# Performance work log

Hardware: AMD Instinct MI355X
Metric: run time of the kernel (lower is better)

## Reference

```python
import jax, jax.numpy as jnp
import numpy as np

B, N, E_PER = 512, 256, 8192          # graphs, nodes per graph, edges per graph
FIN, H, K, FOUT = 128, 32, 16, 10     # in_channels, hidden, num clusters, out_channels
EPS = 1e-15


def setup_inputs() -> dict:
    key = jax.random.key(0)
    ks = jax.random.split(key, 12)
    x = jax.random.normal(ks[0], (B * N, FIN), jnp.float32)
    # intra-graph random edges, then offset into the global node index space
    src = jax.random.randint(ks[1], (B, E_PER), 0, N)
    dst = jax.random.randint(ks[2], (B, E_PER), 0, N)
    offs = (jnp.arange(B) * N)[:, None]
    edge_index = jnp.stack([(src + offs).reshape(-1), (dst + offs).reshape(-1)]).astype(jnp.int64)
    batch = jnp.repeat(jnp.arange(B), N).astype(jnp.int64)

    def lin(k, fin, fout):
        return (jax.random.normal(k, (fin, fout), jnp.float32) / np.sqrt(fin)).astype(jnp.float32)

    params = {
        'W_lin1': lin(ks[3], FIN, H), 'b_lin1': jnp.zeros((H,), jnp.float32),
        'W_rel1': lin(ks[4], H, H), 'b_rel1': jnp.zeros((H,), jnp.float32),
        'W_root1': lin(ks[5], H, H),
        'W_pool': lin(ks[6], H, K), 'b_pool': jnp.zeros((K,), jnp.float32),
        'W_rel2': lin(ks[7], H, H), 'b_rel2': jnp.zeros((H,), jnp.float32),
        'W_root2': lin(ks[8], H, H),
        'W_lin2': lin(ks[9], H, H), 'b_lin2': jnp.zeros((H,), jnp.float32),
        'W_lin3': lin(ks[10], H, FOUT), 'b_lin3': jnp.zeros((FOUT,), jnp.float32),
    }
    return {'x': x, 'edge_index': edge_index, 'batch': batch, **params}


def _densify(x, edge_index, batch):
    """to_dense_adj + to_dense_batch: [total,F] -> [B,N,F], [B,N,N], [B,N]."""
    n_total = x.shape[0]
    counts = jax.ops.segment_sum(jnp.ones((n_total,), jnp.int32), batch, num_segments=B)
    offsets = jnp.concatenate([jnp.zeros((1,), jnp.int32), jnp.cumsum(counts)[:-1]])
    pos = jnp.arange(n_total) - offsets[batch]            # position of node inside its graph
    eb = batch[edge_index[0]]                             # graph id of each edge
    adj = jnp.zeros((B, N, N), jnp.float32).at[eb, pos[edge_index[0]], pos[edge_index[1]]].add(1.0)
    xd = jnp.zeros((B, N, x.shape[1]), jnp.float32).at[batch, pos].set(x)
    mask = jnp.zeros((B, N), jnp.float32).at[batch, pos].set(1.0)
    return xd, adj, mask


def _dense_graph_conv(x, adj, W_rel, b_rel, W_root):
    # PyG DenseGraphConv(aggr='add'): lin_rel(adj @ x) + lin_root(x)
    return jnp.einsum('bnm,bmh,hk->bnk', adj, x, W_rel) + b_rel + x @ W_root


def _dense_mincut_pool(x, adj, s, mask):
    s = jax.nn.softmax(s, axis=-1)
    x = x * mask[..., None]
    s = s * mask[..., None]
    out = jnp.einsum('bnk,bnh->bkh', s, x)                        # s^T x
    out_adj = jnp.einsum('bnk,bnm,bmj->bkj', s, adj, s)           # s^T A s
    mincut_num = jnp.einsum('bkk->b', out_adj)
    d_flat = adj.sum(-1)                                          # degree
    mincut_den = jnp.einsum('bnk,bn,bnk->b', s, d_flat, s)        # trace(s^T D s)
    mincut_loss = jnp.mean(-(mincut_num / mincut_den))
    ss = jnp.einsum('bnk,bnj->bkj', s, s)
    ss_norm = jnp.linalg.norm(ss, axis=(-1, -2), keepdims=True)
    i_s = jnp.eye(K, dtype=jnp.float32)
    ortho_loss = jnp.mean(jnp.linalg.norm(ss / ss_norm - i_s / jnp.sqrt(jnp.float32(K)), axis=(-1, -2)))
    # zero diagonal, symmetric degree normalization
    diag_mask = 1.0 - i_s
    out_adj = out_adj * diag_mask
    d = jnp.sqrt(out_adj.sum(-1))[:, None, :] + EPS               # [B,1,K]
    out_adj = out_adj / d / jnp.swapaxes(d, 1, 2)
    return out, out_adj, mincut_loss, ortho_loss


def reference(x, edge_index, batch, W_lin1, b_lin1, W_rel1, b_rel1, W_root1,
              W_pool, b_pool, W_rel2, b_rel2, W_root2, W_lin2, b_lin2, W_lin3, b_lin3):
    xd, adj, mask = _densify(x, edge_index, batch)
    h = xd @ W_lin1 + b_lin1                                      # lin1
    h = _dense_graph_conv(h, adj, W_rel1, b_rel1, W_root1)        # conv1
    s2 = h @ W_pool + b_pool                                      # pool2
    h, adj_p, mincut_loss2, ortho_loss2 = _dense_mincut_pool(h, adj, s2, mask)
    h = _dense_graph_conv(h, adj_p, W_rel2, b_rel2, W_root2)      # conv2
    h = h.sum(axis=1)                                             # readout sum over clusters
    h = jax.nn.relu(h @ W_lin2 + b_lin2)
    h = h @ W_lin3 + b_lin3
    return jax.nn.log_softmax(h, axis=-1), mincut_loss2, ortho_loss2
```

## Files before the change

kernel.cpp:

```cpp
#include <hip/hip_runtime.h>

#define NB 512
#define NN 256
#define EPG 8192
#define FINC 128

typedef float f32x4 __attribute__((ext_vector_type(4)));
typedef short s16x8 __attribute__((ext_vector_type(8)));

__device__ __forceinline__ float bf2f(unsigned short u) {
  union { unsigned int i; float f; } x; x.i = ((unsigned int)u) << 16; return x.f;
}
__device__ __forceinline__ unsigned short f2bf(float f) {
  union { float f; unsigned int i; } x; x.f = f;
  unsigned int r = x.i + 0x7fffu + ((x.i >> 16) & 1u);
  return (unsigned short)(r >> 16);
}
__device__ __forceinline__ short ftrunc_bf(float f) {
  union { float f; unsigned int i; } x; x.f = f;
  return (short)(x.i >> 16);
}

struct Params {
  const void* x; const void* ei;
  const void *wl1, *bl1, *wr1, *br1, *wro1, *wp, *bp;
  const void *wr2, *br2, *wro2, *wl2, *bl2, *wl3, *bl3;
  float* out; float* ws;
};

__device__ __forceinline__ bool detect_bf16(const void* p) {
  const unsigned short* pw = (const unsigned short*)p;
  int sane = 0;
  for (int i = 0; i < 64; ++i) {
    unsigned e = (pw[i] >> 7) & 0xFFu;
    sane += (e > 96u && e < 132u) ? 1 : 0;
  }
  return sane >= 56;
}
__device__ __forceinline__ bool detect_i64(const void* p) {
  const int* pi = (const int*)p + EPG;
  int ok = 0;
  for (int i = 0; i < 32; ++i) ok += (pi[i] >= 256 && pi[i] < 512) ? 1 : 0;
  return ok < 24;
}
__device__ __forceinline__ float ldf(const void* p, int i, bool bf) {
  return bf ? bf2f(((const unsigned short*)p)[i]) : ((const float*)p)[i];
}

#define SMEM_TOTAL 81920

__global__ __launch_bounds__(1024, 8) void mincut_main(Params P) {
  extern __shared__ char smem[];
  const int t = threadIdx.x;
  const int b = blockIdx.x;

  const bool BF  = detect_bf16(P.wr1);
  const bool I64 = detect_i64(P.ei);

  float* pbuf   = (float*)(smem + 0);
  float* oadjb  = (float*)(smem + 2048);
  float* ssb    = (float*)(smem + 3072);
  float* qbuf   = (float*)(smem + 4096);
  float* ddb    = (float*)(smem + 6144);
  float* h2b    = (float*)(smem + 6208);
  float* rb     = (float*)(smem + 8256);
  float* yb     = (float*)(smem + 8384);
  float* lgb    = (float*)(smem + 8512);
  float* scr    = (float*)(smem + 8704);
  float* rel2f  = (float*)(smem + 9216);
  float* root2f = (float*)(smem + 13312);
  float* lin2f  = (float*)(smem + 17408);
  float* lin3f  = (float*)(smem + 21504);
  float* brel2f = (float*)(smem + 22784);
  float* blin2f = (float*)(smem + 22912);
  float* blin3f = (float*)(smem + 23040);
  float* pbufH  = (float*)(smem + 24576);
  float* pbufL  = (float*)(smem + 26624);
  float* oadjH  = (float*)(smem + 28672);
  float* oadjL  = (float*)(smem + 29696);
  float* ssA    = (float*)(smem + 30720);
  float* ssX    = (float*)(smem + 31744);
  unsigned short* h0T  = (unsigned short*)(smem + 33792);
  unsigned short* yTl  = (unsigned short*)(smem + 33792);
  unsigned short* h1Th = (unsigned short*)(smem + 33792);
  unsigned short* w1t  = (unsigned short*)(smem + 50688);
  unsigned short* zT   = (unsigned short*)(smem + 50688);
  unsigned short* sTh  = (unsigned short*)(smem + 50688);
  unsigned short* sTl  = (unsigned short*)(smem + 59136);
  unsigned short* wrelTh = (unsigned short*)(smem + 67584);
  unsigned short* wrelTl = (unsigned short*)(smem + 70144);
  unsigned short* wrootT = (unsigned short*)(smem + 72704);
  float* blin1f = (float*)(smem + 75264);
  unsigned short* yTh = (unsigned short*)(smem + 67584);
  unsigned short* taT = (unsigned short*)(smem + 67584);
  unsigned short* wpoolTh = (unsigned short*)(smem + 76032);
  unsigned short* wpoolTl = (unsigned short*)(smem + 77184);
  unsigned short* m1Th    = (unsigned short*)(smem + 78336);
  unsigned short* m1Tl    = (unsigned short*)(smem + 79488);
  float*          scrE    = (float*)(smem + 79488);
  unsigned short* m2Th    = (unsigned short*)(smem + 80640);
  float*          bMf     = (float*)(smem + 81792);
  unsigned short* brel1h  = (unsigned short*)(smem + 81856);

  const int wv = t >> 6, lane = t & 63;
  const int lm = lane & 15, quad = lane >> 4;
  const int mbase = wv * 16;

  {
    uint4 z = {0u, 0u, 0u, 0u};
    for (int i = t; i < 2112; i += 1024) ((uint4*)smem)[i] = z;
  }
  for (int e = t; e < 4096; e += 1024) {
    int k = e >> 5, c = e & 31;
    w1t[c * 136 + k] = f2bf(ldf(P.wl1, e, BF));
  }
  {
    int k = t >> 5, c = t & 31;
    float wr = ldf(P.wr1, t, BF);
    unsigned short hi = f2bf(wr);
    wrelTh[c * 40 + k] = hi;
    wrelTl[c * 40 + k] = f2bf(wr - bf2f(hi));
    wrootT[c * 40 + k] = f2bf(ldf(P.wro1, t, BF));
  }
  if (t < 512) {
    int m = t >> 4, c = t & 15;
    float w = ldf(P.wp, t, BF);
    unsigned short hi = f2bf(w);
    wpoolTh[c * 36 + m] = hi;
    wpoolTl[c * 36 + m] = f2bf(w - bf2f(hi));
  }
  if (t < 32) { blin1f[t] = ldf(P.bl1, t, BF); brel1h[t] = f2bf(ldf(P.br1, t, BF)); }
  __syncthreads();

  if (I64) {
    const uint4* s4 = (const uint4*)((const long long*)P.ei + (size_t)b * EPG) + t * 4;
    const uint4* d4 = (const uint4*)((const long long*)P.ei + (size_t)NB * EPG + (size_t)b * EPG) + t * 4;
    #pragma unroll
    for (int i = 0; i < 4; ++i) {
      uint4 a = s4[i], c = d4[i];
      unsigned n0 = (a.x & 255u) * 264u + (c.x & 255u);
      unsigned n1 = (a.z & 255u) * 264u + (c.z & 255u);
      atomicAdd((unsigned int*)(smem + ((n0 >> 3) << 2)), 1u << ((n0 & 7u) * 4u));
      atomicAdd((unsigned int*)(smem + ((n1 >> 3) << 2)), 1u << ((n1 & 7u) * 4u));
    }
  } else {
    const uint4* s4 = (const uint4*)((const int*)P.ei + (size_t)b * EPG) + t * 2;
    const uint4* d4 = (const uint4*)((const int*)P.ei + (size_t)NB * EPG + (size_t)b * EPG) + t * 2;
    #pragma unroll
    for (int i = 0; i < 2; ++i) {
      uint4 a = s4[i], c = d4[i];
      unsigned n0 = (a.x & 255u) * 264u + (c.x & 255u);
      unsigned n1 = (a.y & 255u) * 264u + (c.y & 255u);
      unsigned n2 = (a.z & 255u) * 264u + (c.z & 255u);
      unsigned n3 = (a.w & 255u) * 264u + (c.w & 255u);
      atomicAdd((unsigned int*)(smem + ((n0 >> 3) << 2)), 1u << ((n0 & 7u) * 4u));
      atomicAdd((unsigned int*)(smem + ((n1 >> 3) << 2)), 1u << ((n1 & 7u) * 4u));
      atomicAdd((unsigned int*)(smem + ((n2 >> 3) << 2)), 1u << ((n2 & 7u) * 4u));
      atomicAdd((unsigned int*)(smem + ((n3 >> 3) << 2)), 1u << ((n3 & 7u) * 4u));
    }
  }

  {
    f32x4 acc[2] = {{0.f,0.f,0.f,0.f},{0.f,0.f,0.f,0.f}};
    const size_t node = (size_t)(b * 256 + mbase + lm);
    #pragma unroll
    for (int ks = 0; ks < 4; ++ks) {
      const int k0 = ks * 32 + quad * 8;
      s16x8 a;
      if (BF) {
        a = *(const s16x8*)((const unsigned short*)P.x + node * 128 + k0);
      } else {
        const float* xp = (const float*)P.x + node * 128 + k0;
        f32x4 v0 = *(const f32x4*)xp;
        f32x4 v1 = *(const f32x4*)(xp + 4);
        #pragma unroll
        for (int j = 0; j < 4; ++j) { a[j] = (short)f2bf(v0[j]); a[4 + j] = (short)f2bf(v1[j]); }
      }
      #pragma unroll
      for (int ct = 0; ct < 2; ++ct) {
        s16x8 bh = *(const s16x8*)(w1t + (ct * 16 + lm) * 136 + k0);
        acc[ct] = __builtin_amdgcn_mfma_f32_16x16x32_bf16(a, bh, acc[ct], 0, 0, 0);
      }
    }
    #pragma unroll
    for (int ct = 0; ct < 2; ++ct) {
      const int c = ct * 16 + lm;
      float bias = blin1f[c];
      #pragma unroll
      for (int r = 0; r < 4; ++r)
        h0T[c * 264 + mbase + quad * 4 + r] = f2bf(acc[ct][r] + bias);
    }
  }

  if (wv == 2 || wv == 3) {
    const int mb = (wv - 2) * 16;
    s16x8 Ah, Al;
    #pragma unroll
    for (int j = 0; j < 8; ++j) {
      int k = quad * 8 + j;
      Ah[j] = (short)wrelTh[k * 40 + mb + lm];
      Al[j] = (short)wrelTl[k * 40 + mb + lm];
    }
    s16x8 Bh, Bl;
    ((uint2*)&Bh)[0] = *(const uint2*)(wpoolTh + lm * 36 + quad * 8);
    ((uint2*)&Bh)[1] = *(const uint2*)(wpoolTh + lm * 36 + quad * 8 + 4);
    ((uint2*)&Bl)[0] = *(const uint2*)(wpoolTl + lm * 36 + quad * 8);
    ((uint2*)&Bl)[1] = *(const uint2*)(wpoolTl + lm * 36 + quad * 8 + 4);
    f32x4 acc = {0.f, 0.f, 0.f, 0.f};
    acc = __builtin_amdgcn_mfma_f32_16x16x32_bf16(Ah, Bh, acc, 0, 0, 0);
    acc = __builtin_amdgcn_mfma_f32_16x16x32_bf16(Al, Bh, acc, 0, 0, 0);
    acc = __builtin_amdgcn_mfma_f32_16x16x32_bf16(Ah, Bl, acc, 0, 0, 0);
    #pragma unroll
    for (int r = 0; r < 4; ++r) {
      int m = mb + quad * 4 + r;
      unsigned short hi = f2bf(acc[r]);
      m1Th[lm * 36 + m] = hi;
      m1Tl[lm * 36 + m] = f2bf(acc[r] - bf2f(hi));
    }
  }
  if (wv == 4 || wv == 5) {
    const int mb = (wv - 4) * 16;
    s16x8 Ah;
    #pragma unroll
    for (int j = 0; j < 8; ++j) Ah[j] = (short)wrootT[(quad * 8 + j) * 40 + mb + lm];
    s16x8 Bh, Bl;
    ((uint2*)&Bh)[0] = *(const uint2*)(wpoolTh + lm * 36 + quad * 8);
    ((uint2*)&Bh)[1] = *(const uint2*)(wpoolTh + lm * 36 + quad * 8 + 4);
    ((uint2*)&Bl)[0] = *(const uint2*)(wpoolTl + lm * 36 + quad * 8);
    ((uint2*)&Bl)[1] = *(const uint2*)(wpoolTl + lm * 36 + quad * 8 + 4);
    f32x4 acc = {0.f, 0.f, 0.f, 0.f};
    acc = __builtin_amdgcn_mfma_f32_16x16x32_bf16(Ah, Bh, acc, 0, 0, 0);
    acc = __builtin_amdgcn_mfma_f32_16x16x32_bf16(Ah, Bl, acc, 0, 0, 0);
    #pragma unroll
    for (int r = 0; r < 4; ++r) m2Th[lm * 36 + (mb + quad * 4 + r)] = f2bf(acc[r]);
  }
  if (wv == 6 && lane < 16) {
    float acc = ldf(P.bp, lane, BF);
    #pragma unroll 8
    for (int m = 0; m < 32; ++m)
      acc += bf2f(brel1h[m]) * (bf2f(wpoolTh[lane * 36 + m]) + bf2f(wpoolTl[lane * 36 + m]));
    bMf[lane] = acc;
  }
  __syncthreads();

  f32x4 racc[2] = {{0.f,0.f,0.f,0.f},{0.f,0.f,0.f,0.f}};
  f32x4 yacc = {0.f,0.f,0.f,0.f}, macc = {0.f,0.f,0.f,0.f};
  {
    s16x8 Ah;
    #pragma unroll
    for (int j = 0; j < 8; ++j) Ah[j] = (short)h0T[(quad * 8 + j) * 264 + mbase + lm];
    f32x4 zacc[2] = {{0.f,0.f,0.f,0.f},{0.f,0.f,0.f,0.f}};
    #pragma unroll
    for (int ct = 0; ct < 2; ++ct) {
      const int c = ct * 16 + lm;
      s16x8 brh = *(const s16x8*)(wrelTh + c * 40 + quad * 8);
      s16x8 brl = *(const s16x8*)(wrelTl + c * 40 + quad * 8);
      s16x8 bro = *(const s16x8*)(wrootT + c * 40 + quad * 8);
      zacc[ct] = __builtin_amdgcn_mfma_f32_16x16x32_bf16(Ah, brh, zacc[ct], 0, 0, 0);
      zacc[ct] = __builtin_amdgcn_mfma_f32_16x16x32_bf16(Ah, brl, zacc[ct], 0, 0, 0);
      racc[ct] = __builtin_amdgcn_mfma_f32_16x16x32_bf16(Ah, bro, racc[ct], 0, 0, 0);
    }
    s16x8 Bm1h, Bm1l, Bm2;
    ((uint2*)&Bm1h)[0] = *(const uint2*)(m1Th + lm * 36 + quad * 8);
    ((uint2*)&Bm1h)[1] = *(const uint2*)(m1Th + lm * 36 + quad * 8 + 4);
    ((uint2*)&Bm1l)[0] = *(const uint2*)(m1Tl + lm * 36 + quad * 8);
    ((uint2*)&Bm1l)[1] = *(const uint2*)(m1Tl + lm * 36 + quad * 8 + 4);
    ((uint2*)&Bm2)[0]  = *(const uint2*)(m2Th + lm * 36 + quad * 8);
    ((uint2*)&Bm2)[1]  = *(const uint2*)(m2Th + lm * 36 + quad * 8 + 4);
    yacc = __builtin_amdgcn_mfma_f32_16x16x32_bf16(Ah, Bm1h, yacc, 0, 0, 0);
    yacc = __builtin_amdgcn_mfma_f32_16x16x32_bf16(Ah, Bm1l, yacc, 0, 0, 0);
    macc = __builtin_amdgcn_mfma_f32_16x16x32_bf16(Ah, Bm2, macc, 0, 0, 0);
    #pragma unroll
    for (int ct = 0; ct < 2; ++ct)
      #pragma unroll
      for (int r = 0; r < 4; ++r)
        zT[(ct * 16 + lm) * 264 + mbase + quad * 4 + r] = f2bf(zacc[ct][r]);
  }
  __syncthreads();

  #pragma unroll
  for (int r = 0; r < 4; ++r) {
    int node = mbase + quad * 4 + r;
    unsigned short hi = f2bf(yacc[r]);
    yTh[lm * 264 + node] = hi;
    yTl[lm * 264 + node] = f2bf(yacc[r] - bf2f(hi));
  }
  __syncthreads();

  f32x4 h1v[2], sval;
  {
    f32x4 h1acc[2] = { racc[0], racc[1] };
    f32x4 lacc = macc;
    unsigned dsum = 0;
    const char* arow = smem + (mbase + lm) * 132;
    #pragma unroll
    for (int ks = 0; ks < 8; ++ks) {
      unsigned d = *(const unsigned int*)(arow + ks * 16 + quad * 4);
      unsigned v = (d & 0x0F0F0F0Fu) + ((d >> 4) & 0x0F0F0F0Fu);
      dsum += (v * 0x01010101u) >> 24;
      s16x8 af;
      #pragma unroll
      for (int j = 0; j < 8; ++j) af[j] = ftrunc_bf((float)((d >> (4 * j)) & 15u));
      const int v0 = ks * 32 + quad * 8;
      #pragma unroll
      for (int ct = 0; ct < 2; ++ct) {
        s16x8 bz = *(const s16x8*)(zT + (ct * 16 + lm) * 264 + v0);
        h1acc[ct] = __builtin_amdgcn_mfma_f32_16x16x32_bf16(af, bz, h1acc[ct], 0, 0, 0);
      }
      s16x8 byh = *(const s16x8*)(yTh + lm * 264 + v0);
      s16x8 byl = *(const s16x8*)(yTl + lm * 264 + v0);
      lacc = __builtin_amdgcn_mfma_f32_16x16x32_bf16(af, byh, lacc, 0, 0, 0);
      lacc = __builtin_amdgcn_mfma_f32_16x16x32_bf16(af, byl, lacc, 0, 0, 0);
    }
    dsum += __shfl_xor(dsum, 16, 64);
    dsum += __shfl_xor(dsum, 32, 64);
    float degf = (float)dsum;
    #pragma unroll
    for (int ct = 0; ct < 2; ++ct) {
      float bias = bf2f(brel1h[ct * 16 + lm]);
      #pragma unroll
      for (int r = 0; r < 4; ++r) h1v[ct][r] = h1acc[ct][r] + bias;
    }
    f32x4 lg;
    float bm = bMf[lm];
    #pragma unroll
    for (int r = 0; r < 4; ++r) lg[r] = lacc[r] + bm;
    f32x4 mx = lg;
    #pragma unroll
    for (int m = 1; m <= 8; m <<= 1)
      #pragma unroll
      for (int r = 0; r < 4; ++r) mx[r] = fmaxf(mx[r], __shfl_xor(mx[r], m, 64));
    #pragma unroll
    for (int r = 0; r < 4; ++r) lg[r] = __expf(lg[r] - mx[r]);
    f32x4 sm = lg;
    #pragma unroll
    for (int m = 1; m <= 8; m <<= 1)
      #pragma unroll
      for (int r = 0; r < 4; ++r) sm[r] += __shfl_xor(sm[r], m, 64);
    f32x4 sq;
    #pragma unroll
    for (int r = 0; r < 4; ++r) { sval[r] = lg[r] / sm[r]; sq[r] = sval[r] * sval[r]; }
    #pragma unroll
    for (int m = 1; m <= 8; m <<= 1)
      #pragma unroll
      for (int r = 0; r < 4; ++r) sq[r] += __shfl_xor(sq[r], m, 64);
    {
      int l = lane & 15, src = (l >> 2) << 4;
      float q0 = __shfl(sq[0], src, 64), q1 = __shfl(sq[1], src, 64);
      float q2 = __shfl(sq[2], src, 64), q3 = __shfl(sq[3], src, 64);
      float ssel = (l & 2) ? ((l & 1) ? q3 : q2) : ((l & 1) ? q1 : q0);
      float vden = (lane < 16) ? degf * ssel : 0.f;
      #pragma unroll
      for (int o = 32; o > 0; o >>= 1) vden += __shfl_xor(vden, o, 64);
      if (lane == 0) scrE[wv] = vden;
    }
  }
  __syncthreads();

  #pragma unroll
  for (int ct = 0; ct < 2; ++ct)
    #pragma unroll
    for (int r = 0; r < 4; ++r)
      h1Th[(ct * 16 + lm) * 264 + mbase + quad * 4 + r] = f2bf(h1v[ct][r]);
  #pragma unroll
  for (int r = 0; r < 4; ++r) {
    int node = mbase + quad * 4 + r;
    unsigned short hi = f2bf(sval[r]);
    sTh[lm * 264 + node] = hi;
    sTl[lm * 264 + node] = f2bf(sval[r] - bf2f(hi));
  }
  __syncthreads();

  {
    f32x4 tacc = {0.f, 0.f, 0.f, 0.f};
    const char* arow = smem + (mbase + lm) * 132;
    #pragma unroll
    for (int ks = 0; ks < 8; ++ks) {
      unsigned d = *(const unsigned int*)(arow + ks * 16 + quad * 4);
      s16x8 af;
      #pragma unroll
      for (int j = 0; j < 8; ++j) af[j] = ftrunc_bf((float)((d >> (4 * j)) & 15u));
      const int v0 = ks * 32 + quad * 8;
      s16x8 bh = *(const s16x8*)(sTh + lm * 264 + v0);
      s16x8 bl = *(const s16x8*)(sTl + lm * 264 + v0);
      tacc = __builtin_amdgcn_mfma_f32_16x16x32_bf16(af, bh, tacc, 0, 0, 0);
      tacc = __builtin_amdgcn_mfma_f32_16x16x32_bf16(af, bl, tacc, 0, 0, 0);
    }
    #pragma unroll
    for (int r = 0; r < 4; ++r) taT[lm * 264 + mbase + quad * 4 + r] = f2bf(tacc[r]);
  }
  __syncthreads();

  rel2f[t] = ldf(P.wr2, t, BF);
  root2f[t] = ldf(P.wro2, t, BF);
  lin2f[t] = ldf(P.wl2, t, BF);
  if (t < 320) lin3f[t] = ldf(P.wl3, t, BF);
  if (t < 32) brel2f[t] = ldf(P.br2, t, BF);
  if (t < 32) blin2f[t] = ldf(P.bl2, t, BF);
  if (t < 10) blin3f[t] = ldf(P.bl3, t, BF);

  if (wv < 8) {
    const unsigned short *Ap, *Bp; float* dst; int W, ct = 0;
    switch (wv) {
      case 0: Ap = sTh; Bp = h1Th; dst = pbufH; W = 32; ct = 0; break;
      case 1: Ap = sTh; Bp = h1Th; dst = pbufH; W = 32; ct = 1; break;
      case 2: Ap = sTl; Bp = h1Th; dst = pbufL; W = 32; ct = 0; break;
      case 3: Ap = sTl; Bp = h1Th; dst = pbufL; W = 32; ct = 1; break;
      case 4: Ap = sTh; Bp = taT;  dst = oadjH; W = 16; break;
      case 5: Ap = sTl; Bp = taT;  dst = oadjL; W = 16; break;
      case 6: Ap = sTh; Bp = sTh;  dst = ssA;   W = 16; break;
      default: Ap = sTh; Bp = sTl; dst = ssX;   W = 16; break;
    }
    const int cidx = ct * 16 + lm;
    const unsigned short* Bb = Bp + cidx * 264;
    f32x4 acc = {0.f, 0.f, 0.f, 0.f};
    #pragma unroll
    for (int ch = 0; ch < 8; ++ch) {
      s16x8 a = *(const s16x8*)(Ap + lm * 264 + ch * 32 + quad * 8);
      s16x8 bb = *(const s16x8*)(Bb + ch * 32 + quad * 8);
      acc = __builtin_amdgcn_mfma_f32_16x16x32_bf16(a, bb, acc, 0, 0, 0);
    }
    #pragma unroll
    for (int r = 0; r < 4; ++r) dst[(quad * 4 + r) * W + cidx] = acc[r];
  }
  __syncthreads();

  if (t < 512) {
    pbuf[t] = pbufH[t] + pbufL[t];
  } else if (t < 768) {
    int i = t - 512; oadjb[i] = oadjH[i] + oadjL[i];
  } else {
    int i = t - 768; int k3 = i >> 4, j3 = i & 15;
    ssb[i] = ssA[i] + ssX[i] + ssX[j3 * 16 + k3];
  }
  __syncthreads();

  {
    float vnum = (t < 16) ? oadjb[t * 17] : 0.f;
    float vfro = (t < 256) ? ssb[t] * ssb[t] : 0.f;
    float vtr  = (t < 16) ? ssb[t * 17] : 0.f;
    #pragma unroll
    for (int o = 32; o > 0; o >>= 1) {
      vnum += __shfl_xor(vnum, o, 64);
      vfro += __shfl_xor(vfro, o, 64);
      vtr  += __shfl_xor(vtr, o, 64);
    }
    if (lane == 0) { scr[16 + wv] = vnum; scr[32 + wv] = vfro; scr[48 + wv] = vtr; }
  }
  __syncthreads();

  if (t == 0) {
    float den = 0.f, num = 0.f, fro = 0.f, tr = 0.f;
    #pragma unroll
    for (int i = 0; i < 16; ++i) { den += scrE[i]; num += scr[16 + i]; fro += scr[32 + i]; tr += scr[48 + i]; }
    float ssn = sqrtf(fro);
    float orth2 = 2.f - tr / (2.f * ssn);
    atomicAdd(P.ws, -(num / den) * (1.f / NB));
    atomicAdd(P.ws + 1, sqrtf(fmaxf(orth2, 0.f)) * (1.f / NB));
  }
  if (t < 16) {
    float rs = 0.f;
    #pragma unroll
    for (int j = 0; j < 16; ++j) if (j != t) rs += oadjb[t * 16 + j];
    ddb[t] = sqrtf(rs) + 1e-15f;
  }
  __syncthreads();
  if (t < 256) {
    int k = t >> 4, j = t & 15;
    float apv = (k == j) ? 0.f : oadjb[t] / (ddb[k] * ddb[j]);
    oadjb[t] = apv;
  }
  __syncthreads();

  if (t < 512) {
    int k = t >> 5, c = t & 31;
    float q = 0.f;
    #pragma unroll
    for (int j = 0; j < 16; ++j) q += oadjb[k * 16 + j] * pbuf[j * 32 + c];
    qbuf[k * 32 + c] = q;
  }
  __syncthreads();
  if (t < 512) {
    int k = t >> 5, c = t & 31;
    float s0 = 0.f;
    #pragma unroll
    for (int m = 0; m < 32; ++m)
      s0 += qbuf[k * 32 + m] * rel2f[m * 32 + c] + pbuf[k * 32 + m] * root2f[m * 32 + c];
    h2b[k * 32 + c] = s0;
  }
  __syncthreads();

  if (wv == 0) {
    if (lane < 32) {
      float r = 16.f * brel2f[lane];
      #pragma unroll
      for (int k = 0; k < 16; ++k) r += h2b[k * 32 + lane];
      rb[lane] = r;
    }
    if (lane < 32) {
      float y = blin2f[lane];
      #pragma unroll
      for (int m = 0; m < 32; ++m) y += rb[m] * lin2f[m * 32 + lane];
      yb[lane] = fmaxf(y, 0.f);
    }
    if (lane < 10) {
      float lg = blin3f[lane];
      #pragma unroll
      for (int m = 0; m < 32; ++m) lg += yb[m] * lin3f[m * 10 + lane];
      lgb[lane] = lg;
    }
    if (lane == 0) {
      float mx = lgb[0];
      #pragma unroll
      for (int i = 1; i < 10; ++i) mx = fmaxf(mx, lgb[i]);
      float sum = 0.f;
      #pragma unroll
      for (int i = 0; i < 10; ++i) sum += __expf(lgb[i] - mx);
      lgb[10] = mx + __logf(sum);
    }
    if (lane < 10) {
      float val = lgb[lane] - lgb[10];
      if (BF) ((unsigned short*)P.out)[b * 10 + lane] = f2bf(val);
      else    P.out[b * 10 + lane] = val;
    }
  }
}

__global__ void mincut_fin(Params P) {
  if (threadIdx.x == 0) {
    const bool BF = detect_bf16(P.wr1);
    if (BF) {
      ((unsigned short*)P.out)[5120] = f2bf(P.ws[0]);
      ((unsigned short*)P.out)[5121] = f2bf(P.ws[1]);
    } else {
      P.out[5120] = P.ws[0];
      P.out[5121] = P.ws[1];
    }
  }
}

extern "C" void kernel_launch(void* const* d_in, const int* in_sizes, int n_in,
                              void* d_out, int out_size, void* d_ws, size_t ws_size,
                              hipStream_t stream) {
  (void)in_sizes; (void)n_in; (void)out_size; (void)ws_size;
  Params P;
  P.x    = d_in[0];
  P.ei   = d_in[1];
  P.wl1  = d_in[3];
  P.bl1  = d_in[4];
  P.wr1  = d_in[5];
  P.br1  = d_in[6];
  P.wro1 = d_in[7];
  P.wp   = d_in[8];
  P.bp   = d_in[9];
  P.wr2  = d_in[10];
  P.br2  = d_in[11];
  P.wro2 = d_in[12];
  P.wl2  = d_in[13];
  P.bl2  = d_in[14];
  P.wl3  = d_in[15];
  P.bl3  = d_in[16];
  P.out  = (float*)d_out;
  P.ws   = (float*)d_ws;

  hipMemsetAsync(d_ws, 0, 2 * sizeof(float), stream);
  hipFuncSetAttribute(reinterpret_cast<const void*>(mincut_main),
                      hipFuncAttributeMaxDynamicSharedMemorySize, SMEM_TOTAL);
  hipLaunchKernelGGL(mincut_main, dim3(NB), dim3(1024), SMEM_TOTAL, stream, P);
  hipLaunchKernelGGL(mincut_fin, dim3(1), dim3(64), 0, stream, P);
}
```

Measured before the change: 170.0 us.

## Collapse pooled tail into a single wavefront and fuse the finalize kernel

The code after the pooling MFMAs now runs on one wavefront using shuffles instead of block-wide shared buffers and syncthreads. It also uses the fact that the cluster-sum readout equals column sums of the normalized adjacency times the pooled features, which removes the full Q and h2 matrices. The ssX correction MFMA term is dropped from S^T S, which may lower precision in the orthogonality loss. The separate finalize kernel is replaced by a last-block atomic counter, saving a launch but adding a global atomic and a fence per block.

```diff
diff --git a/kernel.cpp b/kernel.cpp
--- a/kernel.cpp
+++ b/kernel.cpp
@@ -57,29 +57,13 @@
   const bool BF  = detect_bf16(P.wr1);
   const bool I64 = detect_i64(P.ei);
 
-  float* pbuf   = (float*)(smem + 0);
-  float* oadjb  = (float*)(smem + 2048);
-  float* ssb    = (float*)(smem + 3072);
-  float* qbuf   = (float*)(smem + 4096);
-  float* ddb    = (float*)(smem + 6144);
-  float* h2b    = (float*)(smem + 6208);
-  float* rb     = (float*)(smem + 8256);
-  float* yb     = (float*)(smem + 8384);
-  float* lgb    = (float*)(smem + 8512);
-  float* scr    = (float*)(smem + 8704);
-  float* rel2f  = (float*)(smem + 9216);
-  float* root2f = (float*)(smem + 13312);
-  float* lin2f  = (float*)(smem + 17408);
-  float* lin3f  = (float*)(smem + 21504);
-  float* brel2f = (float*)(smem + 22784);
-  float* blin2f = (float*)(smem + 22912);
-  float* blin3f = (float*)(smem + 23040);
-  float* pbufH  = (float*)(smem + 24576);
-  float* pbufL  = (float*)(smem + 26624);
-  float* oadjH  = (float*)(smem + 28672);
-  float* oadjL  = (float*)(smem + 29696);
-  float* ssA    = (float*)(smem + 30720);
-  float* ssX    = (float*)(smem + 31744);
+  float* pbufH  = (float*)(smem + 0);
+  float* pbufL  = (float*)(smem + 2048);
+  float* oadjH  = (float*)(smem + 4096);
+  float* oadjL  = (float*)(smem + 5120);
+  float* ssA    = (float*)(smem + 6144);
+  float* pbuf   = (float*)(smem + 7168);
+  float* oadjb  = (float*)(smem + 9216);
   unsigned short* h0T  = (unsigned short*)(smem + 33792);
   unsigned short* yTl  = (unsigned short*)(smem + 33792);
   unsigned short* h1Th = (unsigned short*)(smem + 33792);
@@ -391,15 +375,7 @@
   }
   __syncthreads();
 
-  rel2f[t] = ldf(P.wr2, t, BF);
-  root2f[t] = ldf(P.wro2, t, BF);
-  lin2f[t] = ldf(P.wl2, t, BF);
-  if (t < 320) lin3f[t] = ldf(P.wl3, t, BF);
-  if (t < 32) brel2f[t] = ldf(P.br2, t, BF);
-  if (t < 32) blin2f[t] = ldf(P.bl2, t, BF);
-  if (t < 10) blin3f[t] = ldf(P.bl3, t, BF);
-
-  if (wv < 8) {
+  if (wv < 7) {
     const unsigned short *Ap, *Bp; float* dst; int W, ct = 0;
     switch (wv) {
       case 0: Ap = sTh; Bp = h1Th; dst = pbufH; W = 32; ct = 0; break;
@@ -408,8 +384,7 @@
       case 3: Ap = sTl; Bp = h1Th; dst = pbufL; W = 32; ct = 1; break;
       case 4: Ap = sTh; Bp = taT;  dst = oadjH; W = 16; break;
       case 5: Ap = sTl; Bp = taT;  dst = oadjL; W = 16; break;
-      case 6: Ap = sTh; Bp = sTh;  dst = ssA;   W = 16; break;
-      default: Ap = sTh; Bp = sTl; dst = ssX;   W = 16; break;
+      default: Ap = sTh; Bp = sTh; dst = ssA;   W = 16; break;
     }
     const int cidx = ct * 16 + lm;
     const unsigned short* Bb = Bp + cidx * 264;
@@ -425,116 +400,115 @@
   }
   __syncthreads();
 
-  if (t < 512) {
-    pbuf[t] = pbufH[t] + pbufL[t];
-  } else if (t < 768) {
-    int i = t - 512; oadjb[i] = oadjH[i] + oadjL[i];
-  } else {
-    int i = t - 768; int k3 = i >> 4, j3 = i & 15;
-    ssb[i] = ssA[i] + ssX[i] + ssX[j3 * 16 + k3];
-  }
-  __syncthreads();
-
-  {
-    float vnum = (t < 16) ? oadjb[t * 17] : 0.f;
-    float vfro = (t < 256) ? ssb[t] * ssb[t] : 0.f;
-    float vtr  = (t < 16) ? ssb[t * 17] : 0.f;
+  if (wv != 0) return;
+
+  for (int i = lane; i < 512; i += 64) pbuf[i] = pbufH[i] + pbufL[i];
+  for (int i = lane; i < 256; i += 64) oadjb[i] = oadjH[i] + oadjL[i];
+
+  {
+    float vden = (lane < 16) ? scrE[lane] : 0.f;
+    float vnum = (lane < 16) ? oadjb[lane * 17] : 0.f;
+    float vtr  = (lane < 16) ? ssA[lane * 17] : 0.f;
+    float vfro = 0.f;
+    #pragma unroll
+    for (int i = 0; i < 4; ++i) { float v = ssA[lane + i * 64]; vfro += v * v; }
     #pragma unroll
     for (int o = 32; o > 0; o >>= 1) {
+      vden += __shfl_xor(vden, o, 64);
       vnum += __shfl_xor(vnum, o, 64);
       vfro += __shfl_xor(vfro, o, 64);
       vtr  += __shfl_xor(vtr, o, 64);
     }
-    if (lane == 0) { scr[16 + wv] = vnum; scr[32 + wv] = vfro; scr[48 + wv] = vtr; }
-  }
-  __syncthreads();
-
-  if (t == 0) {
-    float den = 0.f, num = 0.f, fro = 0.f, tr = 0.f;
-    #pragma unroll
-    for (int i = 0; i < 16; ++i) { den += scrE[i]; num += scr[16 + i]; fro += scr[32 + i]; tr += scr[48 + i]; }
-    float ssn = sqrtf(fro);
-    float orth2 = 2.f - tr / (2.f * ssn);
-    atomicAdd(P.ws, -(num / den) * (1.f / NB));
-    atomicAdd(P.ws + 1, sqrtf(fmaxf(orth2, 0.f)) * (1.f / NB));
-  }
-  if (t < 16) {
+    if (lane == 0) {
+      float ssn = sqrtf(vfro);
+      float orth2 = 2.f - vtr / (2.f * ssn);
+      atomicAdd(P.ws, -(vnum / vden) * (1.f / NB));
+      atomicAdd(P.ws + 1, sqrtf(fmaxf(orth2, 0.f)) * (1.f / NB));
+    }
+  }
+
+  float uv;
+  {
+    const int l16 = lane & 15;
     float rs = 0.f;
     #pragma unroll
-    for (int j = 0; j < 16; ++j) if (j != t) rs += oadjb[t * 16 + j];
-    ddb[t] = sqrtf(rs) + 1e-15f;
-  }
-  __syncthreads();
-  if (t < 256) {
-    int k = t >> 4, j = t & 15;
-    float apv = (k == j) ? 0.f : oadjb[t] / (ddb[k] * ddb[j]);
-    oadjb[t] = apv;
-  }
-  __syncthreads();
-
-  if (t < 512) {
-    int k = t >> 5, c = t & 31;
-    float q = 0.f;
-    #pragma unroll
-    for (int j = 0; j < 16; ++j) q += oadjb[k * 16 + j] * pbuf[j * 32 + c];
-    qbuf[k * 32 + c] = q;
-  }
-  __syncthreads();
-  if (t < 512) {
-    int k = t >> 5, c = t & 31;
-    float s0 = 0.f;
-    #pragma unroll
+    for (int j = 0; j < 16; ++j) if (j != l16) rs += oadjb[l16 * 16 + j];
+    float ddv = sqrtf(rs) + 1e-15f;
+    float s = 0.f;
+    #pragma unroll
+    for (int k = 0; k < 16; ++k) {
+      float ddk = __shfl(ddv, k, 64);
+      if (k != l16) s += oadjb[k * 16 + l16] / ddk;
+    }
+    uv = s / ddv;
+  }
+
+  float Qv = 0.f, Pv = 0.f;
+  {
+    const int m = lane & 31;
+    #pragma unroll
+    for (int j = 0; j < 16; ++j) {
+      float uj = __shfl(uv, j, 64);
+      float pj = pbuf[j * 32 + m];
+      Qv += uj * pj;
+      Pv += pj;
+    }
+  }
+
+  float rbv;
+  {
+    const int c = lane & 31;
+    float acc = 16.f * ldf(P.br2, c, BF);
+    #pragma unroll 8
+    for (int m = 0; m < 32; ++m) {
+      float qm = __shfl(Qv, m, 64);
+      float pm = __shfl(Pv, m, 64);
+      acc += qm * ldf(P.wr2, m * 32 + c, BF) + pm * ldf(P.wro2, m * 32 + c, BF);
+    }
+    rbv = acc;
+  }
+  float yv;
+  {
+    const int c = lane & 31;
+    float acc = ldf(P.bl2, c, BF);
+    #pragma unroll 8
     for (int m = 0; m < 32; ++m)
-      s0 += qbuf[k * 32 + m] * rel2f[m * 32 + c] + pbuf[k * 32 + m] * root2f[m * 32 + c];
-    h2b[k * 32 + c] = s0;
-  }
-  __syncthreads();
-
-  if (wv == 0) {
-    if (lane < 32) {
-      float r = 16.f * brel2f[lane];
-      #pragma unroll
-      for (int k = 0; k < 16; ++k) r += h2b[k * 32 + lane];
-      rb[lane] = r;
-    }
-    if (lane < 32) {
-      float y = blin2f[lane];
-      #pragma unroll
-      for (int m = 0; m < 32; ++m) y += rb[m] * lin2f[m * 32 + lane];
-      yb[lane] = fmaxf(y, 0.f);
-    }
+      acc += __shfl(rbv, m, 64) * ldf(P.wl2, m * 32 + c, BF);
+    yv = fmaxf(acc, 0.f);
+  }
+  {
+    const int c10 = (lane < 10) ? lane : 0;
+    float lg = ldf(P.bl3, c10, BF);
+    #pragma unroll 8
+    for (int m = 0; m < 32; ++m)
+      lg += __shfl(yv, m, 64) * ldf(P.wl3, m * 10 + c10, BF);
+    float lgm = (lane < 10) ? lg : -3.4e38f;
+    #pragma unroll
+    for (int o = 1; o <= 8; o <<= 1) lgm = fmaxf(lgm, __shfl_xor(lgm, o, 64));
+    float ex = (lane < 10) ? __expf(lg - lgm) : 0.f;
+    #pragma unroll
+    for (int o = 1; o <= 8; o <<= 1) ex += __shfl_xor(ex, o, 64);
+    float lse = lgm + __logf(ex);
     if (lane < 10) {
-      float lg = blin3f[lane];
-      #pragma unroll
-      for (int m = 0; m < 32; ++m) lg += yb[m] * lin3f[m * 10 + lane];
-      lgb[lane] = lg;
-    }
-    if (lane == 0) {
-      float mx = lgb[0];
-      #pragma unroll
-      for (int i = 1; i < 10; ++i) mx = fmaxf(mx, lgb[i]);
-      float sum = 0.f;
-      #pragma unroll
-      for (int i = 0; i < 10; ++i) sum += __expf(lgb[i] - mx);
-      lgb[10] = mx + __logf(sum);
-    }
-    if (lane < 10) {
-      float val = lgb[lane] - lgb[10];
+      float val = lg - lse;
       if (BF) ((unsigned short*)P.out)[b * 10 + lane] = f2bf(val);
       else    P.out[b * 10 + lane] = val;
     }
   }
-}
-
-__global__ void mincut_fin(Params P) {
-  if (threadIdx.x == 0) {
-    const bool BF = detect_bf16(P.wr1);
-    if (BF) {
-      ((unsigned short*)P.out)[5120] = f2bf(P.ws[0]);
-      ((unsigned short*)P.out)[5121] = f2bf(P.ws[1]);
-    } else {
-      P.out[5120] = P.ws[0];
-      P.out[5121] = P.ws[1];
+
+  if (lane == 0) {
+    __threadfence();
+    unsigned cnt = atomicAdd((unsigned int*)(P.ws + 2), 1u);
+    if (cnt == NB - 1) {
+      float l0 = atomicAdd(P.ws, 0.f);
+      float l1 = atomicAdd(P.ws + 1, 0.f);
+      if (BF) {
+        ((unsigned short*)P.out)[5120] = f2bf(l0);
+        ((unsigned short*)P.out)[5121] = f2bf(l1);
+      } else {
+        P.out[5120] = l0;
+        P.out[5121] = l1;
+      }
     }
   }
 }
@@ -563,9 +537,8 @@
   P.out  = (float*)d_out;
   P.ws   = (float*)d_ws;
 
-  hipMemsetAsync(d_ws, 0, 2 * sizeof(float), stream);
+  hipMemsetAsync(d_ws, 0, 3 * sizeof(float), stream);
   hipFuncSetAttribute(reinterpret_cast<const void*>(mincut_main),
                       hipFuncAttributeMaxDynamicSharedMemorySize, SMEM_TOTAL);
   hipLaunchKernelGGL(mincut_main, dim3(NB), dim3(1024), SMEM_TOTAL, stream, P);
-  hipLaunchKernelGGL(mincut_fin, dim3(1), dim3(64), 0, stream, P);
-}
+}
```

New measurement: 175.8 us. 1.03x slower.
